# Kernel optimization log

Measured on AMD Instinct MI355X. Metric: run time of the kernel, lower is better.

Reference implementation:

```python
import jax, jax.numpy as jnp
import numpy as np

B, N, DEG = 256, 16384, 32  # batch, num_neurons, fan-in per neuron

def setup_inputs() -> dict:
    key = jax.random.key(0)
    kx, kw, ki = jax.random.split(key, 3)
    x = jax.random.normal(kx, (B, N), dtype=jnp.float32)
    w = jax.random.normal(kw, (N, DEG), dtype=jnp.float32)  # nonzero weights per neuron
    idx = jax.random.randint(ki, (N, DEG), 0, N)            # source-neuron indices per neuron
    return {"x": x, "w": w, "idx": idx}

def reference(x, w, idx):
    # Per neuron j: gather its fan-in channels and apply Dense(1) with
    # kernel = nonzero weights, then relu; concat over neurons == axis N.
    gathered = x[:, idx]                      # [B, N, DEG] gather
    out = jnp.einsum('bnd,nd->bn', gathered, w)  # sparse matvec per batch row
    return jax.nn.relu(out)                   # [B, N]
```

## Files before the change

### kernel.cpp

```cpp
#include <hip/hip_runtime.h>


#define B      256
#define N      16384
#define DEG    32
#define NT     32
#define NCHUNK 8
#define CB     32

typedef float v4f __attribute__((ext_vector_type(4)));
typedef _Float16 h4 __attribute__((ext_vector_type(4)));

__global__ __launch_bounds__(256) void chunk_transpose_f16_kernel(
    const float* __restrict__ x, _Float16* __restrict__ xc) {
    __shared__ float tile[64][65];
    const int t  = threadIdx.x;
    const int j0 = blockIdx.x * 64;
    const int b0 = blockIdx.y * 64;
    const int c4 = t & 15;
    const int r  = t >> 4;

#pragma unroll
    for (int it = 0; it < 4; ++it) {
        const int row = r + it * 16;
        const float4 v = *(const float4*)&x[(size_t)(b0 + row) * N + j0 + 4 * c4];
        tile[row][4 * c4 + 0] = v.x;
        tile[row][4 * c4 + 1] = v.y;
        tile[row][4 * c4 + 2] = v.z;
        tile[row][4 * c4 + 3] = v.w;
    }
    __syncthreads();

    const int wv = t >> 6, l = t & 63;
    const int rl = l >> 3;
    const int a  = l & 7;

#pragma unroll
    for (int it = 0; it < 4; ++it) {
        const int q  = wv * 4 + it;
        const int R  = q * 8 + rl;
        const int cl = R >> 6;
        const int j  = R & 63;
        h4 h;
        h.x = (_Float16)tile[cl * 32 + 4 * a + 0][j];
        h.y = (_Float16)tile[cl * 32 + 4 * a + 1][j];
        h.z = (_Float16)tile[cl * 32 + 4 * a + 2][j];
        h.w = (_Float16)tile[cl * 32 + 4 * a + 3][j];
        *(h4*)&xc[(size_t)((b0 >> 5) + cl) * N * CB + (size_t)(j0 + j) * CB + 4 * a] = h;
    }
}

__global__ __launch_bounds__(256, 8) void gather_dot_f16_kernel(
    const _Float16* __restrict__ xc, const float* __restrict__ w,
    const int* __restrict__ idx, float* __restrict__ out) {
    __shared__ __align__(16) float smem[2048];
    int*   sidx = (int*)smem;
    float* sw   = smem + NT * DEG;

    const int t     = threadIdx.x;
    const int chunk = blockIdx.x & 7;
    const int nb    = (int)(blockIdx.x >> 3) * NT;
    const int wv    = t >> 6;
    const int l     = t & 63;
    const int slot  = wv * 8 + (l >> 3);
    const int a     = l & 7;

    ((int4*)sidx)[t] = ((const int4*)(idx + (size_t)nb * DEG))[t];
    ((float4*)sw)[t] = ((const float4*)(w   + (size_t)nb * DEG))[t];
    __syncthreads();

    const _Float16* xcb = xc + (size_t)chunk * N * CB + 4 * a;
    const int4*   sidx4 = (const int4*)sidx;
    const float4* sw4   = (const float4*)sw;

    float4 acc = make_float4(0.f, 0.f, 0.f, 0.f);
#pragma unroll
    for (int d4 = 0; d4 < DEG / 4; ++d4) {
        const int4   j4 = sidx4[slot * (DEG / 4) + d4];
        const float4 w4 = sw4[slot * (DEG / 4) + d4];
        const h4 v0 = *(const h4*)&xcb[(size_t)j4.x * CB];
        const h4 v1 = *(const h4*)&xcb[(size_t)j4.y * CB];
        const h4 v2 = *(const h4*)&xcb[(size_t)j4.z * CB];
        const h4 v3 = *(const h4*)&xcb[(size_t)j4.w * CB];
        acc.x = fmaf(w4.x, (float)v0.x, acc.x); acc.y = fmaf(w4.x, (float)v0.y, acc.y);
        acc.z = fmaf(w4.x, (float)v0.z, acc.z); acc.w = fmaf(w4.x, (float)v0.w, acc.w);
        acc.x = fmaf(w4.y, (float)v1.x, acc.x); acc.y = fmaf(w4.y, (float)v1.y, acc.y);
        acc.z = fmaf(w4.y, (float)v1.z, acc.z); acc.w = fmaf(w4.y, (float)v1.w, acc.w);
        acc.x = fmaf(w4.z, (float)v2.x, acc.x); acc.y = fmaf(w4.z, (float)v2.y, acc.y);
        acc.z = fmaf(w4.z, (float)v2.z, acc.z); acc.w = fmaf(w4.z, (float)v2.w, acc.w);
        acc.x = fmaf(w4.w, (float)v3.x, acc.x); acc.y = fmaf(w4.w, (float)v3.y, acc.y);
        acc.z = fmaf(w4.w, (float)v3.z, acc.z); acc.w = fmaf(w4.w, (float)v3.w, acc.w);
    }
    __syncthreads();

    float* tile = smem;
    tile[slot * 33 + 4 * a + 0] = acc.x;
    tile[slot * 33 + 4 * a + 1] = acc.y;
    tile[slot * 33 + 4 * a + 2] = acc.z;
    tile[slot * 33 + 4 * a + 3] = acc.w;
    __syncthreads();

    const int br = wv * 8 + (l >> 3);
    const int n0 = 4 * (l & 7);
    v4f v;
    v.x = fmaxf(tile[(n0 + 0) * 33 + br], 0.f);
    v.y = fmaxf(tile[(n0 + 1) * 33 + br], 0.f);
    v.z = fmaxf(tile[(n0 + 2) * 33 + br], 0.f);
    v.w = fmaxf(tile[(n0 + 3) * 33 + br], 0.f);
    __builtin_nontemporal_store(v, (v4f*)&out[(size_t)(chunk * CB + br) * N + nb + n0]);
}

extern "C" void kernel_launch(void* const* d_in, const int* in_sizes, int n_in,
                              void* d_out, int out_size, void* d_ws, size_t ws_size,
                              hipStream_t stream) {
    const float* x   = (const float*)d_in[0];
    const float* w   = (const float*)d_in[1];
    const int*   idx = (const int*)d_in[2];
    float* out = (float*)d_out;
    _Float16* xc = (_Float16*)d_ws;

    dim3 tgrid(N / 64, B / 64);
    chunk_transpose_f16_kernel<<<tgrid, 256, 0, stream>>>(x, xc);

    gather_dot_f16_kernel<<<(N / NT) * NCHUNK, 256, 0, stream>>>(xc, w, idx, out);
}
```

Measured before the change: 98.02 us.

## Widen batch chunks to 64 so each gather loads 128-bit half8 rows

Changes the chunked fp16 layout of x from 8 chunks of 32 batch rows to 4 chunks of 64, so each gathered source neuron yields a 16-byte load per lane covering 8 batch values instead of 8 bytes. This halves the number of gather-kernel blocks and halves how often idx and w are re-read per chunk. Each thread now keeps 8 accumulators. The index and weight shared-memory tiles are transposed so that reads are by d4-major rows, and the output transpose is reworked to write 64 batch rows per block. It costs more registers per thread and gives fewer blocks in flight.

```diff
diff --git a/kernel.cpp b/kernel.cpp
--- a/kernel.cpp
+++ b/kernel.cpp
@@ -5,25 +5,25 @@
 #define N      16384
 #define DEG    32
 #define NT     32
-#define NCHUNK 8
-#define CB     32
+#define NCHUNK 4
+#define CB     64
 
 typedef float v4f __attribute__((ext_vector_type(4)));
-typedef _Float16 h4 __attribute__((ext_vector_type(4)));
+typedef _Float16 h8v __attribute__((ext_vector_type(8)));
 
 __global__ __launch_bounds__(256) void chunk_transpose_f16_kernel(
     const float* __restrict__ x, _Float16* __restrict__ xc) {
     __shared__ float tile[64][65];
-    const int t  = threadIdx.x;
-    const int j0 = blockIdx.x * 64;
-    const int b0 = blockIdx.y * 64;
+    const int t     = threadIdx.x;
+    const int j0    = blockIdx.x * 64;
+    const int chunk = blockIdx.y;
     const int c4 = t & 15;
     const int r  = t >> 4;
 
 #pragma unroll
     for (int it = 0; it < 4; ++it) {
         const int row = r + it * 16;
-        const float4 v = *(const float4*)&x[(size_t)(b0 + row) * N + j0 + 4 * c4];
+        const float4 v = *(const float4*)&x[(size_t)(chunk * 64 + row) * N + j0 + 4 * c4];
         tile[row][4 * c4 + 0] = v.x;
         tile[row][4 * c4 + 1] = v.y;
         tile[row][4 * c4 + 2] = v.z;
@@ -32,82 +32,79 @@
     __syncthreads();
 
     const int wv = t >> 6, l = t & 63;
-    const int rl = l >> 3;
     const int a  = l & 7;
-
+    _Float16* dst = xc + (size_t)chunk * N * CB + 8 * a;
 #pragma unroll
-    for (int it = 0; it < 4; ++it) {
-        const int q  = wv * 4 + it;
-        const int R  = q * 8 + rl;
-        const int cl = R >> 6;
-        const int j  = R & 63;
-        h4 h;
-        h.x = (_Float16)tile[cl * 32 + 4 * a + 0][j];
-        h.y = (_Float16)tile[cl * 32 + 4 * a + 1][j];
-        h.z = (_Float16)tile[cl * 32 + 4 * a + 2][j];
-        h.w = (_Float16)tile[cl * 32 + 4 * a + 3][j];
-        *(h4*)&xc[(size_t)((b0 >> 5) + cl) * N * CB + (size_t)(j0 + j) * CB + 4 * a] = h;
+    for (int p = 0; p < 2; ++p) {
+        const int j = p * 32 + wv * 8 + (l >> 3);
+        h8v h;
+#pragma unroll
+        for (int k = 0; k < 8; ++k) h[k] = (_Float16)tile[8 * a + k][j];
+        *(h8v*)&dst[(size_t)(j0 + j) * CB] = h;
     }
 }
 
 __global__ __launch_bounds__(256, 8) void gather_dot_f16_kernel(
     const _Float16* __restrict__ xc, const float* __restrict__ w,
     const int* __restrict__ idx, float* __restrict__ out) {
-    __shared__ __align__(16) float smem[2048];
+    __shared__ __align__(16) float smem[64 * 33];
     int*   sidx = (int*)smem;
-    float* sw   = smem + NT * DEG;
+    float* sw   = smem + 1024;
 
     const int t     = threadIdx.x;
-    const int chunk = blockIdx.x & 7;
-    const int nb    = (int)(blockIdx.x >> 3) * NT;
+    const int chunk = blockIdx.x & 3;
+    const int nb    = (int)(blockIdx.x >> 2) * NT;
     const int wv    = t >> 6;
     const int l     = t & 63;
     const int slot  = wv * 8 + (l >> 3);
     const int a     = l & 7;
 
-    ((int4*)sidx)[t] = ((const int4*)(idx + (size_t)nb * DEG))[t];
-    ((float4*)sw)[t] = ((const float4*)(w   + (size_t)nb * DEG))[t];
+    {
+        const int n_l = t >> 3, d4 = t & 7;
+        ((int4*)sidx)[d4 * 32 + n_l] = ((const int4*)(idx + (size_t)nb * DEG))[t];
+        ((float4*)sw)[d4 * 32 + n_l] = ((const float4*)(w + (size_t)nb * DEG))[t];
+    }
     __syncthreads();
 
-    const _Float16* xcb = xc + (size_t)chunk * N * CB + 4 * a;
-    const int4*   sidx4 = (const int4*)sidx;
-    const float4* sw4   = (const float4*)sw;
+    const _Float16* xcb = xc + (size_t)chunk * N * CB + 8 * a;
 
-    float4 acc = make_float4(0.f, 0.f, 0.f, 0.f);
+    float acc[8] = {0.f, 0.f, 0.f, 0.f, 0.f, 0.f, 0.f, 0.f};
 #pragma unroll
     for (int d4 = 0; d4 < DEG / 4; ++d4) {
-        const int4   j4 = sidx4[slot * (DEG / 4) + d4];
-        const float4 w4 = sw4[slot * (DEG / 4) + d4];
-        const h4 v0 = *(const h4*)&xcb[(size_t)j4.x * CB];
-        const h4 v1 = *(const h4*)&xcb[(size_t)j4.y * CB];
-        const h4 v2 = *(const h4*)&xcb[(size_t)j4.z * CB];
-        const h4 v3 = *(const h4*)&xcb[(size_t)j4.w * CB];
-        acc.x = fmaf(w4.x, (float)v0.x, acc.x); acc.y = fmaf(w4.x, (float)v0.y, acc.y);
-        acc.z = fmaf(w4.x, (float)v0.z, acc.z); acc.w = fmaf(w4.x, (float)v0.w, acc.w);
-        acc.x = fmaf(w4.y, (float)v1.x, acc.x); acc.y = fmaf(w4.y, (float)v1.y, acc.y);
-        acc.z = fmaf(w4.y, (float)v1.z, acc.z); acc.w = fmaf(w4.y, (float)v1.w, acc.w);
-        acc.x = fmaf(w4.z, (float)v2.x, acc.x); acc.y = fmaf(w4.z, (float)v2.y, acc.y);
-        acc.z = fmaf(w4.z, (float)v2.z, acc.z); acc.w = fmaf(w4.z, (float)v2.w, acc.w);
-        acc.x = fmaf(w4.w, (float)v3.x, acc.x); acc.y = fmaf(w4.w, (float)v3.y, acc.y);
-        acc.z = fmaf(w4.w, (float)v3.z, acc.z); acc.w = fmaf(w4.w, (float)v3.w, acc.w);
+        const int4   j4 = ((const int4*)sidx)[d4 * 32 + slot];
+        const float4 w4 = ((const float4*)sw)[d4 * 32 + slot];
+        const h8v v0 = *(const h8v*)&xcb[(size_t)j4.x * CB];
+        const h8v v1 = *(const h8v*)&xcb[(size_t)j4.y * CB];
+        const h8v v2 = *(const h8v*)&xcb[(size_t)j4.z * CB];
+        const h8v v3 = *(const h8v*)&xcb[(size_t)j4.w * CB];
+#pragma unroll
+        for (int k = 0; k < 8; ++k) acc[k] = fmaf(w4.x, (float)v0[k], acc[k]);
+#pragma unroll
+        for (int k = 0; k < 8; ++k) acc[k] = fmaf(w4.y, (float)v1[k], acc[k]);
+#pragma unroll
+        for (int k = 0; k < 8; ++k) acc[k] = fmaf(w4.z, (float)v2[k], acc[k]);
+#pragma unroll
+        for (int k = 0; k < 8; ++k) acc[k] = fmaf(w4.w, (float)v3[k], acc[k]);
     }
     __syncthreads();
 
     float* tile = smem;
-    tile[slot * 33 + 4 * a + 0] = acc.x;
-    tile[slot * 33 + 4 * a + 1] = acc.y;
-    tile[slot * 33 + 4 * a + 2] = acc.z;
-    tile[slot * 33 + 4 * a + 3] = acc.w;
+#pragma unroll
+    for (int k = 0; k < 8; ++k)
+        tile[(8 * a + k) * 33 + slot] = acc[k];
     __syncthreads();
 
-    const int br = wv * 8 + (l >> 3);
-    const int n0 = 4 * (l & 7);
-    v4f v;
-    v.x = fmaxf(tile[(n0 + 0) * 33 + br], 0.f);
-    v.y = fmaxf(tile[(n0 + 1) * 33 + br], 0.f);
-    v.z = fmaxf(tile[(n0 + 2) * 33 + br], 0.f);
-    v.w = fmaxf(tile[(n0 + 3) * 33 + br], 0.f);
-    __builtin_nontemporal_store(v, (v4f*)&out[(size_t)(chunk * CB + br) * N + nb + n0]);
+#pragma unroll
+    for (int p = 0; p < 2; ++p) {
+        const int b = wv * 16 + p * 8 + (l >> 3);
+        const int c = l & 7;
+        v4f v;
+        v.x = fmaxf(tile[b * 33 + 4 * c + 0], 0.f);
+        v.y = fmaxf(tile[b * 33 + 4 * c + 1], 0.f);
+        v.z = fmaxf(tile[b * 33 + 4 * c + 2], 0.f);
+        v.w = fmaxf(tile[b * 33 + 4 * c + 3], 0.f);
+        __builtin_nontemporal_store(v, (v4f*)&out[(size_t)(chunk * CB + b) * N + nb + 4 * c]);
+    }
 }
 
 extern "C" void kernel_launch(void* const* d_in, const int* in_sizes, int n_in,
```

Result: faster. 90.86 us (-7.3%).
